# Kernel tuning notes

Measured on AMD Instinct MI355X. Metric: run time of the kernel, lower is better.

Reference implementation:

```python
import jax, jax.numpy as jnp
import numpy as np

N, M, D = 8192, 8192, 256
EPS = 1e-7
NEG = -1e9


def setup_inputs() -> dict:
    key = jax.random.key(0)
    k1, k2, k3, k4 = jax.random.split(key, 4)
    xi = jax.random.normal(k1, (N, D), dtype=jnp.float32)
    xj = jax.random.normal(k2, (M, D), dtype=jnp.float32)
    # adjacency mask: random binary, int constant w.r.t. grads
    adj = jax.random.randint(k3, (N, M), 0, 2, dtype=jnp.int32)
    beta = jax.random.uniform(k4, (1,), dtype=jnp.float32)  # uniform(0,1) init
    return {"xi": xi, "xj": xj, "adj": adj, "beta": beta}


def reference(xi, xj, adj, beta):
    # row L2 norms -> outer product of norms (N, M)
    xi_n = jnp.linalg.norm(xi, axis=1, keepdims=True)        # (N, 1)
    xj_n = jnp.linalg.norm(xj, axis=1, keepdims=True).T      # (1, M)
    cos = beta * (xi @ xj.T) / (xi_n * xj_n + EPS)           # (N, M)
    mask = (1.0 - adj.astype(cos.dtype)) * NEG
    P = jax.nn.softmax(cos + mask, axis=1)                   # (N, M)
    return P @ xj                                            # (N, D)
```

## Files before the change

### kernel.cpp

```cpp
#include <hip/hip_runtime.h>
#include <hip/hip_bf16.h>


typedef _Float16 half8  __attribute__((ext_vector_type(8)));
typedef _Float16 half4v __attribute__((ext_vector_type(4)));
typedef __fp16   fp16x2 __attribute__((ext_vector_type(2)));
typedef float    f32x16 __attribute__((ext_vector_type(16)));
typedef int      i32x4  __attribute__((ext_vector_type(4)));
typedef unsigned long long u64;

#define GAS __attribute__((address_space(1)))
#define LAS __attribute__((address_space(3)))

#define N_ROWS 8192
#define M_ROWS 8192
#define DDIM   256

__global__ void prep_scale(const float* __restrict__ x, _Float16* __restrict__ xs,
                           const float* __restrict__ betap) {
    int row  = blockIdx.x * 4 + (threadIdx.x >> 6);
    int lane = threadIdx.x & 63;
    const float4 v = *(const float4*)(x + (size_t)row * DDIM + lane * 4);
    float ss = v.x * v.x + v.y * v.y + v.z * v.z + v.w * v.w;
#pragma unroll
    for (int o = 32; o > 0; o >>= 1) ss += __shfl_xor(ss, o, 64);
    float sc = betap[0] / sqrtf(ss);
    half4v hv = {(_Float16)(v.x * sc), (_Float16)(v.y * sc),
                 (_Float16)(v.z * sc), (_Float16)(v.w * sc)};
    *(half4v*)(xs + (size_t)row * DDIM + lane * 4) = hv;
}

__global__ void prep_xj(const float* __restrict__ xj, half8* __restrict__ xjA,
                        half8* __restrict__ xjF) {
    __shared__ _Float16 tileR[32][272];
    __shared__ _Float16 tileN[32][272];
    __shared__ float red[32][8];
    __shared__ float rsc[32];
    const int t  = threadIdx.x;
    const int jb = blockIdx.x;
    const int row = t >> 3, seg = t & 7;
    const float* src = xj + (size_t)(jb * 32 + row) * DDIM + seg * 32;
    float4 v[8];
    float ss = 0.f;
#pragma unroll
    for (int q = 0; q < 8; ++q) {
        v[q] = ((const float4*)src)[q];
        ss += v[q].x * v[q].x + v[q].y * v[q].y + v[q].z * v[q].z + v[q].w * v[q].w;
    }
    red[row][seg] = ss;
    __syncthreads();
    if (t < 32) {
        float s = 0.f;
#pragma unroll
        for (int q = 0; q < 8; ++q) s += red[t][q];
        rsc[t] = 1.0f / sqrtf(s);
    }
    __syncthreads();
    const float sc = rsc[row];
#pragma unroll
    for (int q = 0; q < 8; ++q) {
        int c = seg * 32 + q * 4;
        tileR[row][c + 0] = (_Float16)v[q].x;
        tileR[row][c + 1] = (_Float16)v[q].y;
        tileR[row][c + 2] = (_Float16)v[q].z;
        tileR[row][c + 3] = (_Float16)v[q].w;
        tileN[row][c + 0] = (_Float16)(v[q].x * sc);
        tileN[row][c + 1] = (_Float16)(v[q].y * sc);
        tileN[row][c + 2] = (_Float16)(v[q].z * sc);
        tileN[row][c + 3] = (_Float16)(v[q].w * sc);
    }
    __syncthreads();
#pragma unroll
    for (int rep = 0; rep < 4; ++rep) {
        int idx = t + rep * 256;
        int kt = idx >> 6, l = idx & 63, il = l & 31, hh = l >> 5;
        half8 val = *(const half8*)&tileN[il][kt * 16 + hh * 8];
        xjA[((size_t)jb * 16 + kt) * 64 + l] = val;
    }
#pragma unroll
    for (int rep = 0; rep < 4; ++rep) {
        int idx = t + rep * 256;
        int f = idx >> 7, s = (idx >> 6) & 1, l = idx & 63, il = l & 31, hh = l >> 5;
        int d = f * 32 + il, jl = s * 16 + hh * 8;
        half8 val;
#pragma unroll
        for (int e = 0; e < 8; ++e) val[e] = tileR[jl + e][d];
        xjF[((size_t)jb * 16 + f * 2 + s) * 64 + l] = val;
    }
}

__global__ void prep_mask(const int* __restrict__ adj, u64* __restrict__ maskW) {
    const int w    = threadIdx.x >> 6;
    const int lane = threadIdx.x & 63;
    const int task = blockIdx.x * 4 + w;
    const int row  = task >> 2;
    const int jq   = task & 3;
    const int* base = adj + (size_t)row * M_ROWS + jq * 2048 + lane * 4;
    i32x4 a[8];
#pragma unroll
    for (int k = 0; k < 8; ++k)
        a[k] = __builtin_nontemporal_load((const i32x4*)(base + k * 256));
    u64 myw = 0;
#pragma unroll
    for (int k = 0; k < 8; ++k) {
        u64 b0 = __ballot(a[k][0] != 0);
        u64 b1 = __ballot(a[k][1] != 0);
        u64 b2 = __ballot(a[k][2] != 0);
        u64 b3 = __ballot(a[k][3] != 0);
        if ((lane >> 2) == k) {
            int q = lane & 3;
            myw = (q == 0) ? b0 : (q == 1) ? b1 : (q == 2) ? b2 : b3;
        }
    }
    if (lane < 32)
        maskW[(size_t)row * 128 + jq * 32 + lane] = myw;
}

__global__ __launch_bounds__(512, 2)
void attn_main(const _Float16* __restrict__ xi_s, const half8* __restrict__ xjA,
               const half8* __restrict__ xjF, const u64* __restrict__ maskW,
               float* __restrict__ part, float* __restrict__ denp) {
    extern __shared__ char lds[];
    const int tid  = threadIdx.x;
    const int w    = tid >> 6;
    const int lane = tid & 63;
    const int il   = lane & 31;
    const int h    = lane >> 5;

    const int bid    = blockIdx.x;
    const int jsplit = bid & 7;
    const int itile  = bid >> 3;
    const int ibase  = itile * 256;
    const int irow   = ibase + w * 32 + il;
    const int j0blk  = jsplit * 32;

    half8 bq[16];
#pragma unroll
    for (int kt = 0; kt < 16; ++kt)
        bq[kt] = *(const half8*)(xi_s + (size_t)irow * DDIM + kt * 16 + h * 8);

    f32x16 acc[8];
#pragma unroll
    for (int f = 0; f < 8; ++f)
#pragma unroll
        for (int r = 0; r < 16; ++r) acc[f][r] = 0.f;
    float rden = 0.f;

    const u64* mrow = maskW + (size_t)irow * 128 + (jsplit >> 1) * 32;
    const int  kbase = (jsplit & 1) * 4;
    const char* gA = (const char*)xjA;
    const char* gF = (const char*)xjF;

#define STAGE(T, B)                                                             \
    {                                                                           \
        const size_t blk = (size_t)(j0blk + (T)) * 16384;                       \
        const char* src = (w < 4 ? gA : gF) + blk + (w & 3) * 4096 + (lane << 4); \
        char* dst = lds + (B) * 32768 + (w < 4 ? 0 : 16384) + (w & 3) * 4096 + (lane << 4); \
        _Pragma("unroll")                                                       \
        for (int k = 0; k < 4; ++k)                                             \
            __builtin_amdgcn_global_load_lds(                                   \
                (const GAS unsigned int*)(src + k * 1024),                      \
                (LAS unsigned int*)(dst + k * 1024), 16, 0, 0);                 \
    }

    STAGE(0, 0);
    STAGE(1, 1);
    u64 cw0 = mrow[kbase * 4 + 0], cw1 = mrow[kbase * 4 + 1];
    u64 cw2 = mrow[kbase * 4 + 2], cw3 = mrow[kbase * 4 + 3];
    u64 nw0 = 0, nw1 = 0, nw2 = 0, nw3 = 0;

    for (int t = 0; t < 32; ++t) {
        if (t >= 31) {
            asm volatile("s_waitcnt vmcnt(0)" ::: "memory");
        } else {
            asm volatile("s_waitcnt vmcnt(4)" ::: "memory");
        }
        __builtin_amdgcn_s_barrier();
        __builtin_amdgcn_sched_barrier(0);

        if ((t & 7) == 0) {
            int k = kbase + (((t >> 3) + 1) & 3);
            nw0 = mrow[k * 4 + 0]; nw1 = mrow[k * 4 + 1];
            nw2 = mrow[k * 4 + 2]; nw3 = mrow[k * 4 + 3];
        }
        if (t < 30) STAGE(t + 2, (t + 2) % 3);

        const char* bufA = lds + (t % 3) * 32768;
        const char* bufF = bufA + 16384;

        f32x16 sacc0, sacc1;
#pragma unroll
        for (int r = 0; r < 16; ++r) { sacc0[r] = 0.f; sacc1[r] = 0.f; }
#pragma unroll
        for (int kt = 0; kt < 16; kt += 2) {
            half8 a0 = *(const half8*)(bufA + kt * 1024 + (lane << 4));
            sacc0 = __builtin_amdgcn_mfma_f32_32x32x16_f16(a0, bq[kt], sacc0, 0, 0, 0);
            half8 a1 = *(const half8*)(bufA + (kt + 1) * 1024 + (lane << 4));
            sacc1 = __builtin_amdgcn_mfma_f32_32x32x16_f16(a1, bq[kt + 1], sacc1, 0, 0, 0);
        }
        const unsigned s0 = 8 * (t & 7) + h;
        unsigned x0 = (unsigned)(cw0 >> s0), x1 = (unsigned)(cw1 >> s0);
        unsigned x2 = (unsigned)(cw2 >> s0), x3 = (unsigned)(cw3 >> s0);
        float wv[16];
#pragma unroll
        for (int r = 0; r < 16; ++r) {
            unsigned xq = (r & 3) == 0 ? x0 : (r & 3) == 1 ? x1 : (r & 3) == 2 ? x2 : x3;
            float e = ((xq >> (2 * (r >> 2))) & 1u) ? __expf(sacc0[r] + sacc1[r]) : 0.f;
            wv[r] = e;
            rden += e;
        }
        int pq[8], qq[8];
#pragma unroll
        for (int q = 0; q < 8; ++q) {
            fp16x2 pp = __builtin_amdgcn_cvt_pkrtz(wv[2 * q], wv[2 * q + 1]);
            pq[q] = __builtin_bit_cast(int, pp);
            qq[q] = __shfl_xor(pq[q], 32, 64);
        }
        i32x4 af0 = {h ? qq[2] : pq[0], h ? qq[3] : pq[1], h ? pq[2] : qq[0], h ? pq[3] : qq[1]};
        i32x4 af1 = {h ? qq[6] : pq[4], h ? qq[7] : pq[5], h ? pq[6] : qq[4], h ? pq[7] : qq[5]};
        half8 afA = __builtin_bit_cast(half8, af0);
        half8 afB = __builtin_bit_cast(half8, af1);

#pragma unroll
        for (int f = 0; f < 8; ++f) {
            half8 b0 = *(const half8*)(bufF + (f * 2 + 0) * 1024 + (lane << 4));
            acc[f] = __builtin_amdgcn_mfma_f32_32x32x16_f16(afA, b0, acc[f], 0, 0, 0);
            half8 b1 = *(const half8*)(bufF + (f * 2 + 1) * 1024 + (lane << 4));
            acc[f] = __builtin_amdgcn_mfma_f32_32x32x16_f16(afB, b1, acc[f], 0, 0, 0);
        }
        if ((t & 7) == 7) { cw0 = nw0; cw1 = nw1; cw2 = nw2; cw3 = nw3; }
    }

    rden += __shfl_xor(rden, 32, 64);
    if (lane < 32) denp[(size_t)jsplit * N_ROWS + ibase + w * 32 + lane] = rden;

    float* prow = part + (size_t)jsplit * ((size_t)N_ROWS * DDIM);
#pragma unroll
    for (int f = 0; f < 8; ++f) {
#pragma unroll
        for (int r = 0; r < 16; ++r) {
            int ir = (r & 3) + 8 * (r >> 2) + 4 * h;
            prow[(size_t)(ibase + w * 32 + ir) * DDIM + f * 32 + il] = acc[f][r];
        }
    }
#undef STAGE
}

__global__ void reduce_out(const float* __restrict__ part, const float* __restrict__ denp,
                           float* __restrict__ out) {
    const int row = blockIdx.x;
    const int d   = threadIdx.x;
    float s = 0.f;
#pragma unroll
    for (int q = 0; q < 8; ++q)
        s += part[((size_t)q * N_ROWS + row) * DDIM + d];
    float dn = 0.f;
#pragma unroll
    for (int q = 0; q < 8; ++q)
        dn += denp[(size_t)q * N_ROWS + row];
    out[(size_t)row * DDIM + d] = s / dn;
}

extern "C" void kernel_launch(void* const* d_in, const int* in_sizes, int n_in,
                              void* d_out, int out_size, void* d_ws, size_t ws_size,
                              hipStream_t stream) {
    const float* xi   = (const float*)d_in[0];
    const float* xj   = (const float*)d_in[1];
    const int*   adj  = (const int*)d_in[2];
    const float* beta = (const float*)d_in[3];
    float* out = (float*)d_out;
    char*  ws  = (char*)d_ws;

    _Float16* xi_s  = (_Float16*)(ws);
    half8*    xjA   = (half8*)(ws + (4u << 20));
    half8*    xjF   = (half8*)(ws + (8u << 20));
    float*    denp  = (float*)(ws + (12u << 20));
    u64*      maskW = (u64*)(ws + (13u << 20));
    float*    part  = (float*)(ws + (24u << 20));

    hipFuncSetAttribute((const void*)attn_main,
                        hipFuncAttributeMaxDynamicSharedMemorySize, 98304);

    prep_scale<<<N_ROWS / 4, 256, 0, stream>>>(xi, xi_s, beta);
    prep_xj<<<M_ROWS / 32, 256, 0, stream>>>(xj, xjA, xjF);
    prep_mask<<<N_ROWS * 4 / 4, 256, 0, stream>>>(adj, maskW);
    attn_main<<<256, 512, 98304, stream>>>(xi_s, xjA, xjF, maskW, part, denp);
    reduce_out<<<N_ROWS, 256, 0, stream>>>(part, denp, out);
}
```

Before: 159.2 us.

## Stage only score operand in LDS, read value operand directly from global

The LDS pipeline now stages only the xj score operand (A layout), using four 16 KB buffers with three tiles in flight instead of three 32 KB buffers holding both operands. The PV-stage xj operand (F layout) is loaded straight from global memory into registers, relying on the cache. s_setprio hints wrap the MFMA loops. This cuts LDS footprint and LDS traffic, but adds global-load latency to the second matmul, which is no longer hidden by the async staging.

```diff
diff --git a/kernel.cpp b/kernel.cpp
--- a/kernel.cpp
+++ b/kernel.cpp
@@ -154,26 +154,28 @@
 #define STAGE(T, B)                                                             \
     {                                                                           \
         const size_t blk = (size_t)(j0blk + (T)) * 16384;                       \
-        const char* src = (w < 4 ? gA : gF) + blk + (w & 3) * 4096 + (lane << 4); \
-        char* dst = lds + (B) * 32768 + (w < 4 ? 0 : 16384) + (w & 3) * 4096 + (lane << 4); \
-        _Pragma("unroll")                                                       \
-        for (int k = 0; k < 4; ++k)                                             \
-            __builtin_amdgcn_global_load_lds(                                   \
-                (const GAS unsigned int*)(src + k * 1024),                      \
-                (LAS unsigned int*)(dst + k * 1024), 16, 0, 0);                 \
+        const char* src = gA + blk + w * 2048 + (lane << 4);                    \
+        char* dst = lds + (B) * 16384 + w * 2048 + (lane << 4);                 \
+        __builtin_amdgcn_global_load_lds((const GAS unsigned int*)(src),        \
+                                         (LAS unsigned int*)(dst), 16, 0, 0);   \
+        __builtin_amdgcn_global_load_lds((const GAS unsigned int*)(src + 1024), \
+                                         (LAS unsigned int*)(dst + 1024), 16, 0, 0); \
     }
 
     STAGE(0, 0);
     STAGE(1, 1);
+    STAGE(2, 2);
     u64 cw0 = mrow[kbase * 4 + 0], cw1 = mrow[kbase * 4 + 1];
     u64 cw2 = mrow[kbase * 4 + 2], cw3 = mrow[kbase * 4 + 3];
     u64 nw0 = 0, nw1 = 0, nw2 = 0, nw3 = 0;
 
     for (int t = 0; t < 32; ++t) {
-        if (t >= 31) {
+        if (t < 30) {
+            asm volatile("s_waitcnt vmcnt(4)" ::: "memory");
+        } else if (t == 30) {
+            asm volatile("s_waitcnt vmcnt(2)" ::: "memory");
+        } else {
             asm volatile("s_waitcnt vmcnt(0)" ::: "memory");
-        } else {
-            asm volatile("s_waitcnt vmcnt(4)" ::: "memory");
         }
         __builtin_amdgcn_s_barrier();
         __builtin_amdgcn_sched_barrier(0);
@@ -183,14 +185,14 @@
             nw0 = mrow[k * 4 + 0]; nw1 = mrow[k * 4 + 1];
             nw2 = mrow[k * 4 + 2]; nw3 = mrow[k * 4 + 3];
         }
-        if (t < 30) STAGE(t + 2, (t + 2) % 3);
-
-        const char* bufA = lds + (t % 3) * 32768;
-        const char* bufF = bufA + 16384;
+        if (t < 29) STAGE(t + 3, (t + 3) & 3);
+
+        const char* bufA = lds + (t & 3) * 16384;
 
         f32x16 sacc0, sacc1;
 #pragma unroll
         for (int r = 0; r < 16; ++r) { sacc0[r] = 0.f; sacc1[r] = 0.f; }
+        __builtin_amdgcn_s_setprio(1);
 #pragma unroll
         for (int kt = 0; kt < 16; kt += 2) {
             half8 a0 = *(const half8*)(bufA + kt * 1024 + (lane << 4));
@@ -198,6 +200,7 @@
             half8 a1 = *(const half8*)(bufA + (kt + 1) * 1024 + (lane << 4));
             sacc1 = __builtin_amdgcn_mfma_f32_32x32x16_f16(a1, bq[kt + 1], sacc1, 0, 0, 0);
         }
+        __builtin_amdgcn_s_setprio(0);
         const unsigned s0 = 8 * (t & 7) + h;
         unsigned x0 = (unsigned)(cw0 >> s0), x1 = (unsigned)(cw1 >> s0);
         unsigned x2 = (unsigned)(cw2 >> s0), x3 = (unsigned)(cw3 >> s0);
@@ -221,13 +224,16 @@
         half8 afA = __builtin_bit_cast(half8, af0);
         half8 afB = __builtin_bit_cast(half8, af1);
 
+        const char* fb = gF + (size_t)(j0blk + t) * 16384 + (lane << 4);
+        __builtin_amdgcn_s_setprio(1);
 #pragma unroll
         for (int f = 0; f < 8; ++f) {
-            half8 b0 = *(const half8*)(bufF + (f * 2 + 0) * 1024 + (lane << 4));
+            half8 b0 = *(const half8*)(fb + (f * 2 + 0) * 1024);
             acc[f] = __builtin_amdgcn_mfma_f32_32x32x16_f16(afA, b0, acc[f], 0, 0, 0);
-            half8 b1 = *(const half8*)(bufF + (f * 2 + 1) * 1024 + (lane << 4));
+            half8 b1 = *(const half8*)(fb + (f * 2 + 1) * 1024);
             acc[f] = __builtin_amdgcn_mfma_f32_32x32x16_f16(afB, b1, acc[f], 0, 0, 0);
         }
+        __builtin_amdgcn_s_setprio(0);
         if ((t & 7) == 7) { cw0 = nw0; cw1 = nw1; cw2 = nw2; cw3 = nw3; }
     }
 
@@ -279,11 +285,11 @@
     float*    part  = (float*)(ws + (24u << 20));
 
     hipFuncSetAttribute((const void*)attn_main,
-                        hipFuncAttributeMaxDynamicSharedMemorySize, 98304);
+                        hipFuncAttributeMaxDynamicSharedMemorySize, 65536);
 
     prep_scale<<<N_ROWS / 4, 256, 0, stream>>>(xi, xi_s, beta);
     prep_xj<<<M_ROWS / 32, 256, 0, stream>>>(xj, xjA, xjF);
     prep_mask<<<N_ROWS * 4 / 4, 256, 0, stream>>>(adj, maskW);
-    attn_main<<<256, 512, 98304, stream>>>(xi_s, xjA, xjF, maskW, part, denp);
+    attn_main<<<256, 512, 65536, stream>>>(xi_s, xjA, xjF, maskW, part, denp);
     reduce_out<<<N_ROWS, 256, 0, stream>>>(part, denp, out);
 }
```

New measurement: 261.3 us. 1.64x slower.

## Process two 32-row tiles per wave to reuse LDS fragments, halve waves

Applied to the files above, without the earlier changes.

Each wave now handles 64 query rows (two 32-row MFMA tiles), so every LDS fragment of xj feeds two MFMAs instead of one. The block shrinks from 512 to 256 threads and the LDS pipeline drops from triple to double buffering with a full vmcnt(0) wait each iteration. Mask words are now loaded in the same iteration they are used instead of prefetched one stage ahead. The aim is less LDS read traffic per MFMA. In exchange, register pressure roughly doubles, only 4 waves per block remain to hide latency, and the shallower pipeline exposes more of the global-load and mask-load latency.

```diff
diff --git a/kernel.cpp b/kernel.cpp
--- a/kernel.cpp
+++ b/kernel.cpp
@@ -116,7 +116,7 @@
         maskW[(size_t)row * 128 + jq * 32 + lane] = myw;
 }
 
-__global__ __launch_bounds__(512, 2)
+__global__ __launch_bounds__(256, 1)
 void attn_main(const _Float16* __restrict__ xi_s, const half8* __restrict__ xjA,
                const half8* __restrict__ xjF, const u64* __restrict__ maskW,
                float* __restrict__ part, float* __restrict__ denp) {
@@ -131,22 +131,26 @@
     const int jsplit = bid & 7;
     const int itile  = bid >> 3;
     const int ibase  = itile * 256;
-    const int irow   = ibase + w * 32 + il;
+    const int irowA  = ibase + w * 64 + il;
+    const int irowB  = irowA + 32;
     const int j0blk  = jsplit * 32;
 
-    half8 bq[16];
-#pragma unroll
-    for (int kt = 0; kt < 16; ++kt)
-        bq[kt] = *(const half8*)(xi_s + (size_t)irow * DDIM + kt * 16 + h * 8);
-
-    f32x16 acc[8];
+    half8 bq0[16], bq1[16];
+#pragma unroll
+    for (int kt = 0; kt < 16; ++kt) {
+        bq0[kt] = *(const half8*)(xi_s + (size_t)irowA * DDIM + kt * 16 + h * 8);
+        bq1[kt] = *(const half8*)(xi_s + (size_t)irowB * DDIM + kt * 16 + h * 8);
+    }
+
+    f32x16 accA[8], accB[8];
 #pragma unroll
     for (int f = 0; f < 8; ++f)
 #pragma unroll
-        for (int r = 0; r < 16; ++r) acc[f][r] = 0.f;
-    float rden = 0.f;
-
-    const u64* mrow = maskW + (size_t)irow * 128 + (jsplit >> 1) * 32;
+        for (int r = 0; r < 16; ++r) { accA[f][r] = 0.f; accB[f][r] = 0.f; }
+    float rdenA = 0.f, rdenB = 0.f;
+
+    const u64* mrowA = maskW + (size_t)irowA * 128 + (jsplit >> 1) * 32;
+    const u64* mrowB = maskW + (size_t)irowB * 128 + (jsplit >> 1) * 32;
     const int  kbase = (jsplit & 1) * 4;
     const char* gA = (const char*)xjA;
     const char* gF = (const char*)xjF;
@@ -154,85 +158,110 @@
 #define STAGE(T, B)                                                             \
     {                                                                           \
         const size_t blk = (size_t)(j0blk + (T)) * 16384;                       \
-        const char* src = (w < 4 ? gA : gF) + blk + (w & 3) * 4096 + (lane << 4); \
-        char* dst = lds + (B) * 32768 + (w < 4 ? 0 : 16384) + (w & 3) * 4096 + (lane << 4); \
+        const char* src = (w < 2 ? gA : gF) + blk + (w & 1) * 8192 + (lane << 4); \
+        char* dst = lds + (B) * 32768 + (w < 2 ? 0 : 16384) + (w & 1) * 8192 + (lane << 4); \
         _Pragma("unroll")                                                       \
-        for (int k = 0; k < 4; ++k)                                             \
+        for (int k = 0; k < 8; ++k)                                             \
             __builtin_amdgcn_global_load_lds(                                   \
                 (const GAS unsigned int*)(src + k * 1024),                      \
                 (LAS unsigned int*)(dst + k * 1024), 16, 0, 0);                 \
     }
 
     STAGE(0, 0);
-    STAGE(1, 1);
-    u64 cw0 = mrow[kbase * 4 + 0], cw1 = mrow[kbase * 4 + 1];
-    u64 cw2 = mrow[kbase * 4 + 2], cw3 = mrow[kbase * 4 + 3];
-    u64 nw0 = 0, nw1 = 0, nw2 = 0, nw3 = 0;
+    u64 cwA0, cwA1, cwA2, cwA3, cwB0, cwB1, cwB2, cwB3;
 
     for (int t = 0; t < 32; ++t) {
-        if (t >= 31) {
-            asm volatile("s_waitcnt vmcnt(0)" ::: "memory");
-        } else {
-            asm volatile("s_waitcnt vmcnt(4)" ::: "memory");
-        }
+        asm volatile("s_waitcnt vmcnt(0)" ::: "memory");
         __builtin_amdgcn_s_barrier();
         __builtin_amdgcn_sched_barrier(0);
 
         if ((t & 7) == 0) {
-            int k = kbase + (((t >> 3) + 1) & 3);
-            nw0 = mrow[k * 4 + 0]; nw1 = mrow[k * 4 + 1];
-            nw2 = mrow[k * 4 + 2]; nw3 = mrow[k * 4 + 3];
-        }
-        if (t < 30) STAGE(t + 2, (t + 2) % 3);
-
-        const char* bufA = lds + (t % 3) * 32768;
+            int k = kbase + (t >> 3);
+            cwA0 = mrowA[k * 4 + 0]; cwA1 = mrowA[k * 4 + 1];
+            cwA2 = mrowA[k * 4 + 2]; cwA3 = mrowA[k * 4 + 3];
+            cwB0 = mrowB[k * 4 + 0]; cwB1 = mrowB[k * 4 + 1];
+            cwB2 = mrowB[k * 4 + 2]; cwB3 = mrowB[k * 4 + 3];
+        }
+        if (t < 31) STAGE(t + 1, (t + 1) & 1);
+
+        const char* bufA = lds + (t & 1) * 32768;
         const char* bufF = bufA + 16384;
 
         f32x16 sacc0, sacc1;
 #pragma unroll
         for (int r = 0; r < 16; ++r) { sacc0[r] = 0.f; sacc1[r] = 0.f; }
 #pragma unroll
-        for (int kt = 0; kt < 16; kt += 2) {
-            half8 a0 = *(const half8*)(bufA + kt * 1024 + (lane << 4));
-            sacc0 = __builtin_amdgcn_mfma_f32_32x32x16_f16(a0, bq[kt], sacc0, 0, 0, 0);
-            half8 a1 = *(const half8*)(bufA + (kt + 1) * 1024 + (lane << 4));
-            sacc1 = __builtin_amdgcn_mfma_f32_32x32x16_f16(a1, bq[kt + 1], sacc1, 0, 0, 0);
+        for (int kt = 0; kt < 16; ++kt) {
+            half8 afr = *(const half8*)(bufA + kt * 1024 + (lane << 4));
+            sacc0 = __builtin_amdgcn_mfma_f32_32x32x16_f16(afr, bq0[kt], sacc0, 0, 0, 0);
+            sacc1 = __builtin_amdgcn_mfma_f32_32x32x16_f16(afr, bq1[kt], sacc1, 0, 0, 0);
         }
         const unsigned s0 = 8 * (t & 7) + h;
-        unsigned x0 = (unsigned)(cw0 >> s0), x1 = (unsigned)(cw1 >> s0);
-        unsigned x2 = (unsigned)(cw2 >> s0), x3 = (unsigned)(cw3 >> s0);
-        float wv[16];
-#pragma unroll
-        for (int r = 0; r < 16; ++r) {
-            unsigned xq = (r & 3) == 0 ? x0 : (r & 3) == 1 ? x1 : (r & 3) == 2 ? x2 : x3;
-            float e = ((xq >> (2 * (r >> 2))) & 1u) ? __expf(sacc0[r] + sacc1[r]) : 0.f;
-            wv[r] = e;
-            rden += e;
-        }
-        int pq[8], qq[8];
-#pragma unroll
-        for (int q = 0; q < 8; ++q) {
-            fp16x2 pp = __builtin_amdgcn_cvt_pkrtz(wv[2 * q], wv[2 * q + 1]);
-            pq[q] = __builtin_bit_cast(int, pp);
-            qq[q] = __shfl_xor(pq[q], 32, 64);
-        }
-        i32x4 af0 = {h ? qq[2] : pq[0], h ? qq[3] : pq[1], h ? pq[2] : qq[0], h ? pq[3] : qq[1]};
-        i32x4 af1 = {h ? qq[6] : pq[4], h ? qq[7] : pq[5], h ? pq[6] : qq[4], h ? pq[7] : qq[5]};
-        half8 afA = __builtin_bit_cast(half8, af0);
-        half8 afB = __builtin_bit_cast(half8, af1);
+        half8 afA0, afB0, afA1, afB1;
+        {
+            unsigned x0 = (unsigned)(cwA0 >> s0), x1 = (unsigned)(cwA1 >> s0);
+            unsigned x2 = (unsigned)(cwA2 >> s0), x3 = (unsigned)(cwA3 >> s0);
+            float wv[16];
+#pragma unroll
+            for (int r = 0; r < 16; ++r) {
+                unsigned xq = (r & 3) == 0 ? x0 : (r & 3) == 1 ? x1 : (r & 3) == 2 ? x2 : x3;
+                float e = ((xq >> (2 * (r >> 2))) & 1u) ? __expf(sacc0[r]) : 0.f;
+                wv[r] = e;
+                rdenA += e;
+            }
+            int pq[8], qq[8];
+#pragma unroll
+            for (int q = 0; q < 8; ++q) {
+                fp16x2 pp = __builtin_amdgcn_cvt_pkrtz(wv[2 * q], wv[2 * q + 1]);
+                pq[q] = __builtin_bit_cast(int, pp);
+                qq[q] = __shfl_xor(pq[q], 32, 64);
+            }
+            i32x4 f0 = {h ? qq[2] : pq[0], h ? qq[3] : pq[1], h ? pq[2] : qq[0], h ? pq[3] : qq[1]};
+            i32x4 f1 = {h ? qq[6] : pq[4], h ? qq[7] : pq[5], h ? pq[6] : qq[4], h ? pq[7] : qq[5]};
+            afA0 = __builtin_bit_cast(half8, f0);
+            afB0 = __builtin_bit_cast(half8, f1);
+        }
+        {
+            unsigned x0 = (unsigned)(cwB0 >> s0), x1 = (unsigned)(cwB1 >> s0);
+            unsigned x2 = (unsigned)(cwB2 >> s0), x3 = (unsigned)(cwB3 >> s0);
+            float wv[16];
+#pragma unroll
+            for (int r = 0; r < 16; ++r) {
+                unsigned xq = (r & 3) == 0 ? x0 : (r & 3) == 1 ? x1 : (r & 3) == 2 ? x2 : x3;
+                float e = ((xq >> (2 * (r >> 2))) & 1u) ? __expf(sacc1[r]) : 0.f;
+                wv[r] = e;
+                rdenB += e;
+            }
+            int pq[8], qq[8];
+#pragma unroll
+            for (int q = 0; q < 8; ++q) {
+                fp16x2 pp = __builtin_amdgcn_cvt_pkrtz(wv[2 * q], wv[2 * q + 1]);
+                pq[q] = __builtin_bit_cast(int, pp);
+                qq[q] = __shfl_xor(pq[q], 32, 64);
+            }
+            i32x4 f0 = {h ? qq[2] : pq[0], h ? qq[3] : pq[1], h ? pq[2] : qq[0], h ? pq[3] : qq[1]};
+            i32x4 f1 = {h ? qq[6] : pq[4], h ? qq[7] : pq[5], h ? pq[6] : qq[4], h ? pq[7] : qq[5]};
+            afA1 = __builtin_bit_cast(half8, f0);
+            afB1 = __builtin_bit_cast(half8, f1);
+        }
 
 #pragma unroll
         for (int f = 0; f < 8; ++f) {
             half8 b0 = *(const half8*)(bufF + (f * 2 + 0) * 1024 + (lane << 4));
-            acc[f] = __builtin_amdgcn_mfma_f32_32x32x16_f16(afA, b0, acc[f], 0, 0, 0);
+            accA[f] = __builtin_amdgcn_mfma_f32_32x32x16_f16(afA0, b0, accA[f], 0, 0, 0);
+            accB[f] = __builtin_amdgcn_mfma_f32_32x32x16_f16(afA1, b0, accB[f], 0, 0, 0);
             half8 b1 = *(const half8*)(bufF + (f * 2 + 1) * 1024 + (lane << 4));
-            acc[f] = __builtin_amdgcn_mfma_f32_32x32x16_f16(afB, b1, acc[f], 0, 0, 0);
-        }
-        if ((t & 7) == 7) { cw0 = nw0; cw1 = nw1; cw2 = nw2; cw3 = nw3; }
-    }
-
-    rden += __shfl_xor(rden, 32, 64);
-    if (lane < 32) denp[(size_t)jsplit * N_ROWS + ibase + w * 32 + lane] = rden;
+            accA[f] = __builtin_amdgcn_mfma_f32_32x32x16_f16(afB0, b1, accA[f], 0, 0, 0);
+            accB[f] = __builtin_amdgcn_mfma_f32_32x32x16_f16(afB1, b1, accB[f], 0, 0, 0);
+        }
+    }
+
+    rdenA += __shfl_xor(rdenA, 32, 64);
+    rdenB += __shfl_xor(rdenB, 32, 64);
+    if (lane < 32) {
+        denp[(size_t)jsplit * N_ROWS + ibase + w * 64 + lane] = rdenA;
+        denp[(size_t)jsplit * N_ROWS + ibase + w * 64 + 32 + lane] = rdenB;
+    }
 
     float* prow = part + (size_t)jsplit * ((size_t)N_ROWS * DDIM);
 #pragma unroll
@@ -240,7 +269,8 @@
 #pragma unroll
         for (int r = 0; r < 16; ++r) {
             int ir = (r & 3) + 8 * (r >> 2) + 4 * h;
-            prow[(size_t)(ibase + w * 32 + ir) * DDIM + f * 32 + il] = acc[f][r];
+            prow[(size_t)(ibase + w * 64 + ir) * DDIM + f * 32 + il] = accA[f][r];
+            prow[(size_t)(ibase + w * 64 + 32 + ir) * DDIM + f * 32 + il] = accB[f][r];
         }
     }
 #undef STAGE
@@ -279,11 +309,11 @@
     float*    part  = (float*)(ws + (24u << 20));
 
     hipFuncSetAttribute((const void*)attn_main,
-                        hipFuncAttributeMaxDynamicSharedMemorySize, 98304);
+                        hipFuncAttributeMaxDynamicSharedMemorySize, 65536);
 
     prep_scale<<<N_ROWS / 4, 256, 0, stream>>>(xi, xi_s, beta);
     prep_xj<<<M_ROWS / 32, 256, 0, stream>>>(xj, xjA, xjF);
     prep_mask<<<N_ROWS * 4 / 4, 256, 0, stream>>>(adj, maskW);
-    attn_main<<<256, 512, 98304, stream>>>(xi_s, xjA, xjF, maskW, part, denp);
+    attn_main<<<256, 256, 65536, stream>>>(xi_s, xjA, xjF, maskW, part, denp);
     reduce_out<<<N_ROWS, 256, 0, stream>>>(part, denp, out);
 }
```

Result: slower. 178.3 us (+12.0%).
